# Performance work log

Hardware: AMD Instinct MI355X
Metric: run time of the kernel (lower is better)

The kernel has to match this reference:

```python
import jax, jax.numpy as jnp
import numpy as np

N_NODES, N_EDGES, N_GRAPHS, EMB_DIM, IMG_DIM, N_TYPES = 50000, 800000, 64, 128, 4096, 30


def gcn_conv(x, W, b, row, col, ew, dis, n):
    # PyG GCNConv: x @ W.T, symmetric-normalized weighted aggregation with self-loops, + bias
    xw = x @ W.T                                            # [N, D]
    norm = dis[row] * ew * dis[col]                          # [E]
    agg = jax.ops.segment_sum(norm[:, None] * xw[row], col, num_segments=n)
    agg = agg + (dis * dis)[:, None] * xw                    # self-loop (weight 1) term
    return agg + b


def setup_inputs() -> dict:
    key = jax.random.key(0)
    ks = jax.random.split(key, 20)
    inp = {
        "images": jax.random.normal(ks[0], (N_GRAPHS, IMG_DIM), jnp.float32),
        "node_types": jax.random.randint(ks[1], (N_NODES,), 0, N_TYPES),
        "edge_index": jax.random.randint(ks[2], (2, N_EDGES), 0, N_NODES),
        "edge_attr": jax.random.uniform(ks[3], (N_EDGES,), jnp.float32),
        "batch": jnp.sort(jax.random.randint(ks[4], (N_NODES,), 0, N_GRAPHS)),
    }
    def lin(k, out_d, in_d):
        s = 1.0 / np.sqrt(in_d)
        kw, kb = jax.random.split(k)
        return (jax.random.uniform(kw, (out_d, in_d), jnp.float32, -s, s),
                jax.random.uniform(kb, (out_d,), jnp.float32, -s, s))
    inp["emb_table"] = jax.random.normal(ks[5], (N_TYPES, EMB_DIM), jnp.float32)
    inp["W_img"], inp["b_img"] = lin(ks[6], IMG_DIM, IMG_DIM)      # frozen image backbone head
    inp["W1"], inp["b1"] = lin(ks[7], EMB_DIM, EMB_DIM)
    inp["W2"], inp["b2"] = lin(ks[8], EMB_DIM, EMB_DIM)
    inp["W3"], inp["b3"] = lin(ks[9], EMB_DIM, EMB_DIM)
    inp["Wi"], inp["bi"] = lin(ks[10], EMB_DIM, IMG_DIM)
    inp["Wc"], inp["bc"] = lin(ks[11], EMB_DIM, IMG_DIM + EMB_DIM)
    return inp


def reference(images, node_types, edge_index, edge_attr, batch, emb_table,
              W_img, b_img, W1, b1, W2, b2, W3, b3, Wi, bi, Wc, bc):
    n = node_types.shape[0]
    B = images.shape[0]
    row, col = edge_index[0], edge_index[1]
    # gcn_norm with self-loops (fill value 1): deg at aggregation endpoint (col)
    deg = jax.ops.segment_sum(edge_attr, col, num_segments=n) + 1.0
    dis = jax.lax.rsqrt(deg)
    # frozen image model (linear stand-in for VGG fc head, output dim 4096)
    xi = images @ W_img.T + b_img                           # [B, 4096]
    # encode_images branch
    oi = xi @ Wi.T + bi
    oi = oi / jnp.linalg.norm(oi, axis=1, keepdims=True)
    # encode_images_with_graphs branch
    xg = emb_table[node_types]                              # [N, D]
    xg = jax.nn.relu(gcn_conv(xg, W1, b1, row, col, edge_attr, dis, n))
    xg = jax.nn.relu(gcn_conv(xg, W2, b2, row, col, edge_attr, dis, n))
    xg = gcn_conv(xg, W3, b3, row, col, edge_attr, dis, n)
    cnt = jax.ops.segment_sum(jnp.ones((n,), xg.dtype), batch, num_segments=B)
    pooled = jax.ops.segment_sum(xg, batch, num_segments=B) / jnp.maximum(cnt, 1.0)[:, None]
    oc = jnp.concatenate([xi, pooled], axis=1) @ Wc.T + bc
    oc = oc / jnp.linalg.norm(oc, axis=1, keepdims=True)
    return (oi, oc)
```

## Files before the change

kernel.cpp:

```cpp
#include <hip/hip_runtime.h>
#include <math.h>

#define NN 50000
#define NE 800000
#define NG 64
#define D 128
#define IMG 4096
#define NT 30
#define CAP 64

#define EBLK (NE / 256)
#define PBLK ((NT * D + 2 * D * 64) / 256)
#define CBLK (64 * IMG / 2 / 256)
#define GBLK ((NN + 63) / 64)
#define AGGBLK ((NN + 7) / 8)
#define KSPLIT 16
#define IMGHALF (64 * KSPLIT / 2)
#define IREDBLK (64 * IMG / 256)

typedef unsigned int uint;
typedef unsigned short ushort;
typedef __attribute__((ext_vector_type(8))) __bf16 bf16x8;
typedef __attribute__((ext_vector_type(4))) float f32x4;

__device__ __forceinline__ uint bf16rne(float f) {
  uint h = __float_as_uint(f);
  return (h + 0x7fffu + ((h >> 16) & 1u)) >> 16;
}
__device__ __forceinline__ uint pack2bf(float a, float b) {
  return bf16rne(a) | (bf16rne(b) << 16);
}
__device__ __forceinline__ float bflo(uint u) { return __uint_as_float(u << 16); }
__device__ __forceinline__ float bfhi(uint u) { return __uint_as_float(u & 0xffff0000u); }



__global__ __launch_bounds__(256) void setup_multi(
    const int* __restrict__ row, const int* __restrict__ col,
    const float* __restrict__ ew, int* __restrict__ cnt, int2* __restrict__ ebuf,
    const float* __restrict__ emb, const float* __restrict__ W1, float* __restrict__ embW,
    const float* __restrict__ W2, const float* __restrict__ W3,
    uint* __restrict__ Wbf2, uint* __restrict__ Wbf3,
    const float* __restrict__ images, uint* __restrict__ imgAbf,
    const int* __restrict__ batch, int* __restrict__ goff) {
  int b = blockIdx.x;
  if (b < EBLK) {
    int e = b * 256 + threadIdx.x;
    if (e < NE) {
      int c = col[e];
      int s = atomicAdd(&cnt[c], 1);
      if (s < CAP) ebuf[((size_t)c << 6) + s] = make_int2(row[e], __float_as_int(ew[e]));
    }
  } else if (b < EBLK + PBLK) {
    int tid = (b - EBLK) * 256 + threadIdx.x;
    if (tid < NT * D) {
      int tt = tid >> 7, nn2 = tid & 127;
      const float* ep = emb + (size_t)tt * D;
      const float* wp = W1 + (size_t)nn2 * D;
      float acc = 0.f;
      for (int k = 0; k < D; k += 4) {
        float4 evv = *(const float4*)(ep + k);
        float4 wvv = *(const float4*)(wp + k);
        acc += evv.x * wvv.x + evv.y * wvv.y + evv.z * wvv.z + evv.w * wvv.w;
      }
      embW[tid] = acc;
    } else if (tid < NT * D + D * 64) {
      int j = tid - NT * D;
      float2 v = ((const float2*)W2)[j];
      Wbf2[j] = pack2bf(v.x, v.y);
    } else {
      int j = tid - NT * D - D * 64;
      float2 v = ((const float2*)W3)[j];
      Wbf3[j] = pack2bf(v.x, v.y);
    }
  } else if (b < EBLK + PBLK + CBLK) {
    int idx = (b - EBLK - PBLK) * 256 + threadIdx.x;
    float2 v = ((const float2*)images)[idx];
    imgAbf[idx] = pack2bf(v.x, v.y);
  } else {
    int g = threadIdx.x;
    if (g <= NG) {
      int lo = 0, hi = NN;
      while (lo < hi) {
        int mid = (lo + hi) >> 1;
        if (batch[mid] < g) lo = mid + 1; else hi = mid;
      }
      goff[g] = lo;
    }
  }
}


__global__ __launch_bounds__(256) void node_dis(const int* __restrict__ cnt,
                                                const int2* __restrict__ ebuf,
                                                float* __restrict__ dis) {
  int lane = threadIdx.x & 63;
  int sub = lane >> 4, fl = lane & 15;
  int node = (blockIdx.x * 4 + (threadIdx.x >> 6)) * 4 + sub;
  if (node >= NN) return;
  int n = min(cnt[node], CAP);
  const int2* eb = ebuf + ((size_t)node << 6);
  float acc = 0.f;
  for (int j = fl; j < n; j += 16) acc += __int_as_float(eb[j].y);
  acc += __shfl_xor(acc, 8);
  acc += __shfl_xor(acc, 4);
  acc += __shfl_xor(acc, 2);
  acc += __shfl_xor(acc, 1);
  if (fl == 0) dis[node] = 1.0f / sqrtf(acc + 1.0f);
}


__global__ __launch_bounds__(512) void lay1_fused(const int* __restrict__ cnt,
                                                  const int2* __restrict__ ebuf,
                                                  const float* __restrict__ dis,
                                                  const int* __restrict__ types,
                                                  const float* __restrict__ embW,
                                                  const float* __restrict__ b1,
                                                  uint* __restrict__ outbf) {
  __shared__ float sE[NT * D];
  __shared__ float sB[D];
  int t = threadIdx.x;
  for (int i = t; i < NT * D; i += 512) sE[i] = embW[i];
  if (t < D) sB[t] = b1[t];
  __syncthreads();
  int wave = t >> 6, lane = t & 63;
  #pragma unroll
  for (int r = 0; r < 4; r++) {
    int node = blockIdx.x * 32 + wave * 4 + r;
    if (node >= NN) continue;
    float ax = sB[2 * lane], ay = sB[2 * lane + 1];
    int n = min(cnt[node], CAP);
    const int2* eb = ebuf + ((size_t)node << 6);
    float disc = dis[node];
    int idx = 0;
    for (; idx + 4 <= n; idx += 4) {
      int4 ra = *(const int4*)(eb + idx);
      int4 rb = *(const int4*)(eb + idx + 2);
      float n0 = dis[ra.x] * __int_as_float(ra.y) * disc;
      float n1 = dis[ra.z] * __int_as_float(ra.w) * disc;
      float n2 = dis[rb.x] * __int_as_float(rb.y) * disc;
      float n3 = dis[rb.z] * __int_as_float(rb.w) * disc;
      float2 e0 = *(const float2*)&sE[types[ra.x] * D + 2 * lane];
      float2 e1 = *(const float2*)&sE[types[ra.z] * D + 2 * lane];
      float2 e2 = *(const float2*)&sE[types[rb.x] * D + 2 * lane];
      float2 e3 = *(const float2*)&sE[types[rb.z] * D + 2 * lane];
      ax = fmaf(n0, e0.x, ax); ay = fmaf(n0, e0.y, ay);
      ax = fmaf(n1, e1.x, ax); ay = fmaf(n1, e1.y, ay);
      ax = fmaf(n2, e2.x, ax); ay = fmaf(n2, e2.y, ay);
      ax = fmaf(n3, e3.x, ax); ay = fmaf(n3, e3.y, ay);
    }
    for (; idx < n; idx++) {
      int2 rr = eb[idx];
      float nm = dis[rr.x] * __int_as_float(rr.y) * disc;
      float2 ev = *(const float2*)&sE[types[rr.x] * D + 2 * lane];
      ax = fmaf(nm, ev.x, ax);
      ay = fmaf(nm, ev.y, ay);
    }
    float dd = disc * disc;
    float2 es = *(const float2*)&sE[types[node] * D + 2 * lane];
    ax = fmaf(dd, es.x, ax);
    ay = fmaf(dd, es.y, ay);
    ax = fmaxf(ax, 0.f);
    ay = fmaxf(ay, 0.f);
    outbf[(size_t)node * 64 + lane] = pack2bf(ax, ay);
  }
}


__device__ __forceinline__ void node_gemm_body(const uint* __restrict__ Abf,
                                               const uint* __restrict__ Wbf,
                                               uint* __restrict__ outbf, int bx,
                                               ushort* __restrict__ tile) {
  int w = threadIdx.x >> 6, lane = threadIdx.x & 63;
  int quad = lane >> 4;
  int m0 = bx * 64 + w * 16;
  int mrow = m0 + (lane & 15);
  int arow = (mrow < NN) ? mrow : 0;
  uint4 afr[4];
  #pragma unroll
  for (int ks = 0; ks < 4; ks++)
    afr[ks] = *(const uint4*)(Abf + (size_t)arow * 64 + ks * 16 + quad * 4);
  f32x4 acc[8] = {};
  #pragma unroll
  for (int nt = 0; nt < 8; nt++) {
    int n = nt * 16 + (lane & 15);
    #pragma unroll
    for (int ks = 0; ks < 4; ks++) {
      union { uint4 u; bf16x8 v; } au, bu;
      au.u = afr[ks];
      bu.u = *(const uint4*)(Wbf + (size_t)n * 64 + ks * 16 + quad * 4);
      acc[nt] = __builtin_amdgcn_mfma_f32_16x16x32_bf16(au.v, bu.v, acc[nt], 0, 0, 0);
    }
  }
  ushort* tw = tile + w * 16 * 136;
  #pragma unroll
  for (int nt = 0; nt < 8; nt++)
    #pragma unroll
    for (int i = 0; i < 4; i++)
      tw[(quad * 4 + i) * 136 + nt * 16 + (lane & 15)] = (ushort)bf16rne(acc[nt][i]);
  __builtin_amdgcn_s_waitcnt(0);
  #pragma unroll
  for (int rep = 0; rep < 4; rep++) {
    int r = rep * 4 + quad;
    int j = lane & 15;
    int node = m0 + r;
    if (node < NN) {
      uint4 v = *(const uint4*)&tw[r * 136 + j * 8];
      *(uint4*)(outbf + (size_t)node * 64 + j * 4) = v;
    }
  }
}


__device__ __forceinline__ void img_mfma_body(const uint* __restrict__ Abf,
                                              const float* __restrict__ W,
                                              float* __restrict__ splitbuf, int bx, int by) {
  int wv = threadIdx.x >> 6, lane = threadIdx.x & 63;
  int quad = lane >> 4;
  int n = bx * 64 + wv * 16 + (lane & 15);
  int k0 = by * 256;
  f32x4 acc[4] = {{0.f, 0.f, 0.f, 0.f}, {0.f, 0.f, 0.f, 0.f},
                  {0.f, 0.f, 0.f, 0.f}, {0.f, 0.f, 0.f, 0.f}};
  const float* wp = W + (size_t)n * IMG + k0 + quad * 16;
  const uint* ap = Abf + (size_t)(lane & 15) * (IMG / 2) + k0 / 2 + quad * 8;
  #pragma unroll
  for (int ss = 0; ss < 4; ss++) {
    float4 w0 = *(const float4*)(wp + ss * 64);
    float4 w1 = *(const float4*)(wp + ss * 64 + 4);
    float4 w2 = *(const float4*)(wp + ss * 64 + 8);
    float4 w3 = *(const float4*)(wp + ss * 64 + 12);
    union { uint4 u; bf16x8 v; } b1u, b2u;
    b1u.u.x = pack2bf(w0.x, w0.y);
    b1u.u.y = pack2bf(w0.z, w0.w);
    b1u.u.z = pack2bf(w1.x, w1.y);
    b1u.u.w = pack2bf(w1.z, w1.w);
    b2u.u.x = pack2bf(w2.x, w2.y);
    b2u.u.y = pack2bf(w2.z, w2.w);
    b2u.u.z = pack2bf(w3.x, w3.y);
    b2u.u.w = pack2bf(w3.z, w3.w);
    #pragma unroll
    for (int mt = 0; mt < 4; mt++) {
      const uint* app = ap + (size_t)mt * 16 * (IMG / 2) + ss * 32;
      union { uint4 u; bf16x8 v; } a1u, a2u;
      a1u.u = *(const uint4*)(app);
      a2u.u = *(const uint4*)(app + 4);
      acc[mt] = __builtin_amdgcn_mfma_f32_16x16x32_bf16(a1u.v, b1u.v, acc[mt], 0, 0, 0);
      acc[mt] = __builtin_amdgcn_mfma_f32_16x16x32_bf16(a2u.v, b2u.v, acc[mt], 0, 0, 0);
    }
  }
  #pragma unroll
  for (int mt = 0; mt < 4; mt++)
    #pragma unroll
    for (int i = 0; i < 4; i++) {
      int m = mt * 16 + quad * 4 + i;
      splitbuf[((size_t)by * 64 + m) * IMG + n] = acc[mt][i];
    }
}


__device__ __forceinline__ void aggregate2_body(const uint* __restrict__ xw,
                                                const int* __restrict__ cnt,
                                                const int2* __restrict__ ebuf,
                                                const float* __restrict__ dis,
                                                const float* __restrict__ bias, int relu,
                                                uint* __restrict__ outbf, int blk) {
  const uint2* xw2 = (const uint2*)xw;
  int wave = threadIdx.x >> 6;
  int lane = threadIdx.x & 63;
  int half = lane >> 5;
  int fl = lane & 31;
  int node = (blk * 4 + wave) * 2 + half;
  if (node >= NN) return;
  float a0 = 0.f, a1 = 0.f, a2 = 0.f, a3 = 0.f;
  int n = min(cnt[node], CAP);
  const int2* eb = ebuf + ((size_t)node << 6);
  float disc = dis[node];
  int idx = 0;
  for (; idx + 8 <= n; idx += 8) {
    int4 ra = *(const int4*)(eb + idx);
    int4 rb = *(const int4*)(eb + idx + 2);
    int4 rc = *(const int4*)(eb + idx + 4);
    int4 rd = *(const int4*)(eb + idx + 6);
    float n0 = dis[ra.x] * __int_as_float(ra.y) * disc;
    float n1 = dis[ra.z] * __int_as_float(ra.w) * disc;
    float n2 = dis[rb.x] * __int_as_float(rb.y) * disc;
    float n3 = dis[rb.z] * __int_as_float(rb.w) * disc;
    float n4 = dis[rc.x] * __int_as_float(rc.y) * disc;
    float n5 = dis[rc.z] * __int_as_float(rc.w) * disc;
    float n6 = dis[rd.x] * __int_as_float(rd.y) * disc;
    float n7 = dis[rd.z] * __int_as_float(rd.w) * disc;
    uint2 u0 = xw2[(size_t)ra.x * 32 + fl];
    uint2 u1 = xw2[(size_t)ra.z * 32 + fl];
    uint2 u2 = xw2[(size_t)rb.x * 32 + fl];
    uint2 u3 = xw2[(size_t)rb.z * 32 + fl];
    uint2 u4 = xw2[(size_t)rc.x * 32 + fl];
    uint2 u5 = xw2[(size_t)rc.z * 32 + fl];
    uint2 u6 = xw2[(size_t)rd.x * 32 + fl];
    uint2 u7 = xw2[(size_t)rd.z * 32 + fl];
    a0 = fmaf(n0, bflo(u0.x), a0); a1 = fmaf(n0, bfhi(u0.x), a1);
    a2 = fmaf(n0, bflo(u0.y), a2); a3 = fmaf(n0, bfhi(u0.y), a3);
    a0 = fmaf(n1, bflo(u1.x), a0); a1 = fmaf(n1, bfhi(u1.x), a1);
    a2 = fmaf(n1, bflo(u1.y), a2); a3 = fmaf(n1, bfhi(u1.y), a3);
    a0 = fmaf(n2, bflo(u2.x), a0); a1 = fmaf(n2, bfhi(u2.x), a1);
    a2 = fmaf(n2, bflo(u2.y), a2); a3 = fmaf(n2, bfhi(u2.y), a3);
    a0 = fmaf(n3, bflo(u3.x), a0); a1 = fmaf(n3, bfhi(u3.x), a1);
    a2 = fmaf(n3, bflo(u3.y), a2); a3 = fmaf(n3, bfhi(u3.y), a3);
    a0 = fmaf(n4, bflo(u4.x), a0); a1 = fmaf(n4, bfhi(u4.x), a1);
    a2 = fmaf(n4, bflo(u4.y), a2); a3 = fmaf(n4, bfhi(u4.y), a3);
    a0 = fmaf(n5, bflo(u5.x), a0); a1 = fmaf(n5, bfhi(u5.x), a1);
    a2 = fmaf(n5, bflo(u5.y), a2); a3 = fmaf(n5, bfhi(u5.y), a3);
    a0 = fmaf(n6, bflo(u6.x), a0); a1 = fmaf(n6, bfhi(u6.x), a1);
    a2 = fmaf(n6, bflo(u6.y), a2); a3 = fmaf(n6, bfhi(u6.y), a3);
    a0 = fmaf(n7, bflo(u7.x), a0); a1 = fmaf(n7, bfhi(u7.x), a1);
    a2 = fmaf(n7, bflo(u7.y), a2); a3 = fmaf(n7, bfhi(u7.y), a3);
  }
  for (; idx + 2 <= n; idx += 2) {
    int4 ra = *(const int4*)(eb + idx);
    float n0 = dis[ra.x] * __int_as_float(ra.y) * disc;
    float n1 = dis[ra.z] * __int_as_float(ra.w) * disc;
    uint2 u0 = xw2[(size_t)ra.x * 32 + fl];
    uint2 u1 = xw2[(size_t)ra.z * 32 + fl];
    a0 = fmaf(n0, bflo(u0.x), a0); a1 = fmaf(n0, bfhi(u0.x), a1);
    a2 = fmaf(n0, bflo(u0.y), a2); a3 = fmaf(n0, bfhi(u0.y), a3);
    a0 = fmaf(n1, bflo(u1.x), a0); a1 = fmaf(n1, bfhi(u1.x), a1);
    a2 = fmaf(n1, bflo(u1.y), a2); a3 = fmaf(n1, bfhi(u1.y), a3);
  }
  if (idx < n) {
    int2 r = eb[idx];
    float nm = dis[r.x] * __int_as_float(r.y) * disc;
    uint2 u = xw2[(size_t)r.x * 32 + fl];
    a0 = fmaf(nm, bflo(u.x), a0);
    a1 = fmaf(nm, bfhi(u.x), a1);
    a2 = fmaf(nm, bflo(u.y), a2);
    a3 = fmaf(nm, bfhi(u.y), a3);
  }
  float dd = disc * disc;
  {
    uint2 u = xw2[(size_t)node * 32 + fl];
    a0 = fmaf(dd, bflo(u.x), a0);
    a1 = fmaf(dd, bfhi(u.x), a1);
    a2 = fmaf(dd, bflo(u.y), a2);
    a3 = fmaf(dd, bfhi(u.y), a3);
  }
  float4 b = *(const float4*)(bias + 4 * fl);
  a0 += b.x; a1 += b.y; a2 += b.z; a3 += b.w;
  if (relu) {
    a0 = fmaxf(a0, 0.f);
    a1 = fmaxf(a1, 0.f);
    a2 = fmaxf(a2, 0.f);
    a3 = fmaxf(a3, 0.f);
  }
  uint2 o;
  o.x = pack2bf(a0, a1);
  o.y = pack2bf(a2, a3);
  ((uint2*)outbf)[(size_t)node * 32 + fl] = o;
}

__global__ __launch_bounds__(256) void gemm2_plus_img(const uint* __restrict__ bufX,
                                                      const uint* __restrict__ wbf2,
                                                      uint* __restrict__ bufB,
                                                      const uint* __restrict__ imgAbf,
                                                      const float* __restrict__ Wimg,
                                                      float* __restrict__ splitbuf) {
  __shared__ ushort tile[4 * 16 * 136];
  int b = blockIdx.x;
  if (b < GBLK) {
    node_gemm_body(bufX, wbf2, bufB, b, tile);
  } else {
    int j = b - GBLK;
    img_mfma_body(imgAbf, Wimg, splitbuf, j & 63, j >> 6);
  }
}

__global__ __launch_bounds__(256) void agg2_plus_img(const uint* __restrict__ bufB,
                                                     const int* __restrict__ cnt,
                                                     const int2* __restrict__ ebuf,
                                                     const float* __restrict__ dis,
                                                     const float* __restrict__ b2,
                                                     uint* __restrict__ bufX,
                                                     const uint* __restrict__ imgAbf,
                                                     const float* __restrict__ Wimg,
                                                     float* __restrict__ splitbuf) {
  int b = blockIdx.x;
  if (b < AGGBLK) {
    aggregate2_body(bufB, cnt, ebuf, dis, b2, 1, bufX, b);
  } else {
    int j = b - AGGBLK;
    img_mfma_body(imgAbf, Wimg, splitbuf, j & 63, 8 + (j >> 6));
  }
}

__global__ __launch_bounds__(256) void gemm3_plus_imgred(const uint* __restrict__ bufX,
                                                         const uint* __restrict__ wbf3,
                                                         uint* __restrict__ bufB,
                                                         const float* __restrict__ splitbuf,
                                                         const float* __restrict__ b_img,
                                                         float* __restrict__ xcat) {
  __shared__ ushort tile[4 * 16 * 136];
  int b = blockIdx.x;
  if (b < GBLK) {
    node_gemm_body(bufX, wbf3, bufB, b, tile);
  } else {
    int idx = (b - GBLK) * 256 + threadIdx.x;
    if (idx < 64 * IMG) {
      float acc = b_img[idx & (IMG - 1)];
      #pragma unroll
      for (int s = 0; s < KSPLIT; s++) acc += splitbuf[(size_t)s * 64 * IMG + idx];
      xcat[(size_t)(idx >> 12) * (IMG + D) + (idx & (IMG - 1))] = acc;
    }
  }
}

__global__ __launch_bounds__(256) void aggregate2(const uint* __restrict__ xw,
                                                  const int* __restrict__ cnt,
                                                  const int2* __restrict__ ebuf,
                                                  const float* __restrict__ dis,
                                                  const float* __restrict__ bias, int relu,
                                                  uint* __restrict__ outbf) {
  aggregate2_body(xw, cnt, ebuf, dis, bias, relu, outbf, blockIdx.x);
}


__device__ __forceinline__ void gemm64_body(const float* __restrict__ A, int lda,
                                            const float* __restrict__ W,
                                            const float* __restrict__ bias,
                                            float* __restrict__ out, int N, int K,
                                            int kChunk, int bx, int by,
                                            float (*xs)[68], float (*ws)[68]) {
  int t = threadIdx.x;
  int n0 = bx * 64;
  int k0 = by * kChunk;
  int kEnd = min(K, k0 + kChunk);
  int tn = t & 15;
  int tm = t >> 4;
  float acc[4][4] = {};
  if (by == 0) {
    #pragma unroll
    for (int ni = 0; ni < 4; ni++) {
      float bv = bias[n0 + tn * 4 + ni];
      #pragma unroll
      for (int mi = 0; mi < 4; mi++) acc[mi][ni] = bv;
    }
  }
  for (int kt = k0; kt < kEnd; kt += 16) {
    int kc = (t & 3) * 4;
    int rr = t >> 2;
    float4 va = *(const float4*)(A + (size_t)rr * lda + kt + kc);
    xs[kc + 0][rr] = va.x; xs[kc + 1][rr] = va.y; xs[kc + 2][rr] = va.z; xs[kc + 3][rr] = va.w;
    float4 vw = *(const float4*)(W + (size_t)(n0 + rr) * K + kt + kc);
    ws[kc + 0][rr] = vw.x; ws[kc + 1][rr] = vw.y; ws[kc + 2][rr] = vw.z; ws[kc + 3][rr] = vw.w;
    __syncthreads();
    #pragma unroll
    for (int k = 0; k < 16; k++) {
      float4 xv = *(const float4*)&xs[k][tm * 4];
      float4 wv = *(const float4*)&ws[k][tn * 4];
      float xm[4] = {xv.x, xv.y, xv.z, xv.w};
      float wn[4] = {wv.x, wv.y, wv.z, wv.w};
      #pragma unroll
      for (int mi = 0; mi < 4; mi++)
        #pragma unroll
        for (int ni = 0; ni < 4; ni++)
          acc[mi][ni] = fmaf(xm[mi], wn[ni], acc[mi][ni]);
    }
    __syncthreads();
  }
  #pragma unroll
  for (int mi = 0; mi < 4; mi++)
    #pragma unroll
    for (int ni = 0; ni < 4; ni++)
      atomicAdd(&out[(size_t)(tm * 4 + mi) * N + n0 + tn * 4 + ni], acc[mi][ni]);
}


__global__ __launch_bounds__(256) void pool_gemm_oi(const uint* __restrict__ xb,
                                                    const int* __restrict__ goff,
                                                    float* __restrict__ xcat,
                                                    const float* __restrict__ Wi,
                                                    const float* __restrict__ bi,
                                                    float* __restrict__ oi_raw) {
  __shared__ float xs[16][68];
  __shared__ float ws[16][68];
  int b = blockIdx.x;
  if (b < 2 * NG) {
    int g = b >> 1;
    int chunk = ((b & 1) << 2) + (threadIdx.x >> 6);
    int fl = threadIdx.x & 63;
    int s = goff[g], e = goff[g + 1];
    float inv = 1.0f / fmaxf((float)(e - s), 1.0f);
    float ax = 0.f, ay = 0.f;
    for (int i = s + chunk; i < e; i += 8) {
      uint u = xb[(size_t)i * 64 + fl];
      ax += bflo(u);
      ay += bfhi(u);
    }
    atomicAdd(&xcat[(size_t)g * (IMG + D) + IMG + 2 * fl], ax * inv);
    atomicAdd(&xcat[(size_t)g * (IMG + D) + IMG + 2 * fl + 1], ay * inv);
  } else {
    int j = b - 2 * NG;
    gemm64_body(xcat, IMG + D, Wi, bi, oi_raw, D, IMG, 128, j & 1, j >> 1, xs, ws);
  }
}

__global__ __launch_bounds__(256) void gemm_oc(const float* __restrict__ xcat,
                                               const float* __restrict__ Wc,
                                               const float* __restrict__ bc,
                                               float* __restrict__ oc_raw) {
  __shared__ float xs[16][68];
  __shared__ float ws[16][68];
  int b = blockIdx.x;
  gemm64_body(xcat, IMG + D, Wc, bc, oc_raw, D, IMG + D, 176, b & 1, b >> 1, xs, ws);
}

__global__ __launch_bounds__(128) void normalize_rows(const float* __restrict__ oi_raw,
                                                      const float* __restrict__ oc_raw,
                                                      float* __restrict__ out) {
  int r = blockIdx.x;
  int t = threadIdx.x;
  const float* src = (r < 64) ? (oi_raw + r * D) : (oc_raw + (r - 64) * D);
  float v = src[t];
  __shared__ float red[128];
  red[t] = v * v;
  __syncthreads();
  for (int s = 64; s > 0; s >>= 1) {
    if (t < s) red[t] += red[t + s];
    __syncthreads();
  }
  out[r * D + t] = v / sqrtf(red[0]);
}


extern "C" void kernel_launch(void* const* d_in, const int* in_sizes, int n_in,
                              void* d_out, int out_size, void* d_ws, size_t ws_size,
                              hipStream_t stream) {
  const float* images = (const float*)d_in[0];
  const int* node_types = (const int*)d_in[1];
  const int* erow = (const int*)d_in[2];
  const int* ecol = erow + NE;
  const float* eattr = (const float*)d_in[3];
  const int* batch = (const int*)d_in[4];
  const float* emb = (const float*)d_in[5];
  const float* W_img = (const float*)d_in[6];
  const float* b_img = (const float*)d_in[7];
  const float* W1 = (const float*)d_in[8];
  const float* b1 = (const float*)d_in[9];
  const float* W2 = (const float*)d_in[10];
  const float* b2 = (const float*)d_in[11];
  const float* W3 = (const float*)d_in[12];
  const float* b3 = (const float*)d_in[13];
  const float* Wi = (const float*)d_in[14];
  const float* bi = (const float*)d_in[15];
  const float* Wc = (const float*)d_in[16];
  const float* bc = (const float*)d_in[17];
  float* out = (float*)d_out;

  char* w = (char*)d_ws;
  auto alloc = [&](size_t bytes) -> void* {
    void* p = (void*)w;
    w += (bytes + 511) & ~(size_t)511;
    return p;
  };
  int* cnt = (int*)alloc((size_t)NN * 4);
  float* xcat = (float*)alloc((size_t)64 * (IMG + D) * 4);
  float* oi_raw = (float*)alloc(64 * D * 4);
  float* oc_raw = (float*)alloc(64 * D * 4);
  size_t zero_bytes = (size_t)(w - (char*)d_ws);
  int* goff = (int*)alloc((NG + 1) * 4);
  float* dis = (float*)alloc(NN * 4);
  float* embW1 = (float*)alloc(NT * D * 4);
  uint* wbf2 = (uint*)alloc(D * 64 * 4);
  uint* wbf3 = (uint*)alloc(D * 64 * 4);
  int2* ebuf = (int2*)alloc((size_t)NN * CAP * 8);
  uint* bufX = (uint*)alloc((size_t)NN * D * 2);
  uint* bufB = (uint*)alloc((size_t)NN * D * 2);
  uint* imgAbf = (uint*)alloc((size_t)64 * IMG * 2);
  float* splitbuf = (float*)alloc((size_t)KSPLIT * 64 * IMG * 4);

  hipMemsetAsync(d_ws, 0, zero_bytes, stream);

  setup_multi<<<EBLK + PBLK + CBLK + 1, 256, 0, stream>>>(
      erow, ecol, eattr, cnt, ebuf, emb, W1, embW1, W2, W3, wbf2, wbf3,
      images, imgAbf, batch, goff);
  node_dis<<<(NN + 15) / 16, 256, 0, stream>>>(cnt, ebuf, dis);
  lay1_fused<<<(NN + 31) / 32, 512, 0, stream>>>(cnt, ebuf, dis, node_types, embW1, b1, bufX);
  gemm2_plus_img<<<GBLK + IMGHALF, 256, 0, stream>>>(bufX, wbf2, bufB, imgAbf, W_img,
                                                     splitbuf);
  agg2_plus_img<<<AGGBLK + IMGHALF, 256, 0, stream>>>(bufB, cnt, ebuf, dis, b2, bufX,
                                                      imgAbf, W_img, splitbuf);
  gemm3_plus_imgred<<<GBLK + IREDBLK, 256, 0, stream>>>(bufX, wbf3, bufB, splitbuf, b_img,
                                                        xcat);
  aggregate2<<<AGGBLK, 256, 0, stream>>>(bufB, cnt, ebuf, dis, b3, 0, bufX);
  pool_gemm_oi<<<2 * NG + 64, 256, 0, stream>>>(bufX, goff, xcat, Wi, bi, oi_raw);
  gemm_oc<<<48, 256, 0, stream>>>(xcat, Wc, bc, oc_raw);
  normalize_rows<<<128, 128, 0, stream>>>(oi_raw, oc_raw, out);
}
```

Measured before the change: 422.6 us.

## Zero-pad edge buckets, atomic degree, reorder fused blocks, split pooling kernel

Degree is now accumulated with float atomics during bucketing, which replaces the per-node reduction kernel with a trivial rsqrt kernel. The edge bucket capacity drops to 48 and the buffer is zeroed, so the aggregation loops can run in fixed 8- or 16-edge chunks with no tail handling. Padded entries point to node 0 with weight zero and contribute nothing. The fused kernels now put the image GEMM blocks first so they are scheduled ahead of the graph blocks. The layer-3 aggregation is fused with the oi GEMM, and pooling moves to its own wider kernel. The cost is a larger memset, extra atomics, and truncation for nodes with more than 48 in-edges, which changes results when such nodes exist.

```diff
diff --git a/kernel.cpp b/kernel.cpp
--- a/kernel.cpp
+++ b/kernel.cpp
@@ -7,7 +7,7 @@
 #define D 128
 #define IMG 4096
 #define NT 30
-#define CAP 64
+#define CAP 48
 
 #define EBLK (NE / 256)
 #define PBLK ((NT * D + 2 * D * 64) / 256)
@@ -37,7 +37,8 @@
 
 __global__ __launch_bounds__(256) void setup_multi(
     const int* __restrict__ row, const int* __restrict__ col,
-    const float* __restrict__ ew, int* __restrict__ cnt, int2* __restrict__ ebuf,
+    const float* __restrict__ ew, int* __restrict__ cnt, float* __restrict__ degf,
+    int2* __restrict__ ebuf,
     const float* __restrict__ emb, const float* __restrict__ W1, float* __restrict__ embW,
     const float* __restrict__ W2, const float* __restrict__ W3,
     uint* __restrict__ Wbf2, uint* __restrict__ Wbf3,
@@ -48,8 +49,10 @@
     int e = b * 256 + threadIdx.x;
     if (e < NE) {
       int c = col[e];
+      float wv = ew[e];
       int s = atomicAdd(&cnt[c], 1);
-      if (s < CAP) ebuf[((size_t)c << 6) + s] = make_int2(row[e], __float_as_int(ew[e]));
+      atomicAdd(&degf[c], wv);
+      if (s < CAP) ebuf[(size_t)c * CAP + s] = make_int2(row[e], __float_as_int(wv));
     }
   } else if (b < EBLK + PBLK) {
     int tid = (b - EBLK) * 256 + threadIdx.x;
@@ -91,22 +94,10 @@
 }
 
 
-__global__ __launch_bounds__(256) void node_dis(const int* __restrict__ cnt,
-                                                const int2* __restrict__ ebuf,
-                                                float* __restrict__ dis) {
-  int lane = threadIdx.x & 63;
-  int sub = lane >> 4, fl = lane & 15;
-  int node = (blockIdx.x * 4 + (threadIdx.x >> 6)) * 4 + sub;
-  if (node >= NN) return;
-  int n = min(cnt[node], CAP);
-  const int2* eb = ebuf + ((size_t)node << 6);
-  float acc = 0.f;
-  for (int j = fl; j < n; j += 16) acc += __int_as_float(eb[j].y);
-  acc += __shfl_xor(acc, 8);
-  acc += __shfl_xor(acc, 4);
-  acc += __shfl_xor(acc, 2);
-  acc += __shfl_xor(acc, 1);
-  if (fl == 0) dis[node] = 1.0f / sqrtf(acc + 1.0f);
+__global__ __launch_bounds__(256) void dis_kernel(const float* __restrict__ degf,
+                                                  float* __restrict__ dis) {
+  int i = blockIdx.x * 256 + threadIdx.x;
+  if (i < NN) dis[i] = 1.0f / sqrtf(degf[i] + 1.0f);
 }
 
 
@@ -130,31 +121,41 @@
     if (node >= NN) continue;
     float ax = sB[2 * lane], ay = sB[2 * lane + 1];
     int n = min(cnt[node], CAP);
-    const int2* eb = ebuf + ((size_t)node << 6);
+    int nc = (n + 7) >> 3;
+    const int2* eb = ebuf + (size_t)node * CAP;
     float disc = dis[node];
-    int idx = 0;
-    for (; idx + 4 <= n; idx += 4) {
-      int4 ra = *(const int4*)(eb + idx);
-      int4 rb = *(const int4*)(eb + idx + 2);
-      float n0 = dis[ra.x] * __int_as_float(ra.y) * disc;
-      float n1 = dis[ra.z] * __int_as_float(ra.w) * disc;
-      float n2 = dis[rb.x] * __int_as_float(rb.y) * disc;
-      float n3 = dis[rb.z] * __int_as_float(rb.w) * disc;
-      float2 e0 = *(const float2*)&sE[types[ra.x] * D + 2 * lane];
-      float2 e1 = *(const float2*)&sE[types[ra.z] * D + 2 * lane];
-      float2 e2 = *(const float2*)&sE[types[rb.x] * D + 2 * lane];
-      float2 e3 = *(const float2*)&sE[types[rb.z] * D + 2 * lane];
-      ax = fmaf(n0, e0.x, ax); ay = fmaf(n0, e0.y, ay);
-      ax = fmaf(n1, e1.x, ax); ay = fmaf(n1, e1.y, ay);
-      ax = fmaf(n2, e2.x, ax); ay = fmaf(n2, e2.y, ay);
-      ax = fmaf(n3, e3.x, ax); ay = fmaf(n3, e3.y, ay);
-    }
-    for (; idx < n; idx++) {
-      int2 rr = eb[idx];
-      float nm = dis[rr.x] * __int_as_float(rr.y) * disc;
-      float2 ev = *(const float2*)&sE[types[rr.x] * D + 2 * lane];
-      ax = fmaf(nm, ev.x, ax);
-      ay = fmaf(nm, ev.y, ay);
+    for (int c = 0; c < nc; c++) {
+      const int2* ep = eb + (c << 3);
+      int4 q0 = *(const int4*)(ep + 0);
+      int4 q1 = *(const int4*)(ep + 2);
+      int4 q2 = *(const int4*)(ep + 4);
+      int4 q3 = *(const int4*)(ep + 6);
+      int t0 = types[q0.x], t1 = types[q0.z], t2 = types[q1.x], t3 = types[q1.z];
+      int t4 = types[q2.x], t5 = types[q2.z], t6 = types[q3.x], t7 = types[q3.z];
+      float m0 = dis[q0.x] * __int_as_float(q0.y) * disc;
+      float m1 = dis[q0.z] * __int_as_float(q0.w) * disc;
+      float m2 = dis[q1.x] * __int_as_float(q1.y) * disc;
+      float m3 = dis[q1.z] * __int_as_float(q1.w) * disc;
+      float m4 = dis[q2.x] * __int_as_float(q2.y) * disc;
+      float m5 = dis[q2.z] * __int_as_float(q2.w) * disc;
+      float m6 = dis[q3.x] * __int_as_float(q3.y) * disc;
+      float m7 = dis[q3.z] * __int_as_float(q3.w) * disc;
+      float2 e0 = *(const float2*)&sE[t0 * D + 2 * lane];
+      float2 e1 = *(const float2*)&sE[t1 * D + 2 * lane];
+      float2 e2 = *(const float2*)&sE[t2 * D + 2 * lane];
+      float2 e3 = *(const float2*)&sE[t3 * D + 2 * lane];
+      float2 e4 = *(const float2*)&sE[t4 * D + 2 * lane];
+      float2 e5 = *(const float2*)&sE[t5 * D + 2 * lane];
+      float2 e6 = *(const float2*)&sE[t6 * D + 2 * lane];
+      float2 e7 = *(const float2*)&sE[t7 * D + 2 * lane];
+      ax = fmaf(m0, e0.x, ax); ay = fmaf(m0, e0.y, ay);
+      ax = fmaf(m1, e1.x, ax); ay = fmaf(m1, e1.y, ay);
+      ax = fmaf(m2, e2.x, ax); ay = fmaf(m2, e2.y, ay);
+      ax = fmaf(m3, e3.x, ax); ay = fmaf(m3, e3.y, ay);
+      ax = fmaf(m4, e4.x, ax); ay = fmaf(m4, e4.y, ay);
+      ax = fmaf(m5, e5.x, ax); ay = fmaf(m5, e5.y, ay);
+      ax = fmaf(m6, e6.x, ax); ay = fmaf(m6, e6.y, ay);
+      ax = fmaf(m7, e7.x, ax); ay = fmaf(m7, e7.y, ay);
     }
     float dd = disc * disc;
     float2 es = *(const float2*)&sE[types[node] * D + 2 * lane];
@@ -257,6 +258,10 @@
     }
 }
 
+
+#define GA(k, s_) uint2 u##k = xw2[(size_t)(s_) * 32 + fl];
+#define FA(k, m_) a0 = fmaf(m_, bflo(u##k.x), a0); a1 = fmaf(m_, bfhi(u##k.x), a1); \
+                  a2 = fmaf(m_, bflo(u##k.y), a2); a3 = fmaf(m_, bfhi(u##k.y), a3);
 
 __device__ __forceinline__ void aggregate2_body(const uint* __restrict__ xw,
                                                 const int* __restrict__ cnt,
@@ -273,66 +278,43 @@
   if (node >= NN) return;
   float a0 = 0.f, a1 = 0.f, a2 = 0.f, a3 = 0.f;
   int n = min(cnt[node], CAP);
-  const int2* eb = ebuf + ((size_t)node << 6);
+  int nc = (n + 15) >> 4;
+  const int2* eb = ebuf + (size_t)node * CAP;
   float disc = dis[node];
-  int idx = 0;
-  for (; idx + 8 <= n; idx += 8) {
-    int4 ra = *(const int4*)(eb + idx);
-    int4 rb = *(const int4*)(eb + idx + 2);
-    int4 rc = *(const int4*)(eb + idx + 4);
-    int4 rd = *(const int4*)(eb + idx + 6);
-    float n0 = dis[ra.x] * __int_as_float(ra.y) * disc;
-    float n1 = dis[ra.z] * __int_as_float(ra.w) * disc;
-    float n2 = dis[rb.x] * __int_as_float(rb.y) * disc;
-    float n3 = dis[rb.z] * __int_as_float(rb.w) * disc;
-    float n4 = dis[rc.x] * __int_as_float(rc.y) * disc;
-    float n5 = dis[rc.z] * __int_as_float(rc.w) * disc;
-    float n6 = dis[rd.x] * __int_as_float(rd.y) * disc;
-    float n7 = dis[rd.z] * __int_as_float(rd.w) * disc;
-    uint2 u0 = xw2[(size_t)ra.x * 32 + fl];
-    uint2 u1 = xw2[(size_t)ra.z * 32 + fl];
-    uint2 u2 = xw2[(size_t)rb.x * 32 + fl];
-    uint2 u3 = xw2[(size_t)rb.z * 32 + fl];
-    uint2 u4 = xw2[(size_t)rc.x * 32 + fl];
-    uint2 u5 = xw2[(size_t)rc.z * 32 + fl];
-    uint2 u6 = xw2[(size_t)rd.x * 32 + fl];
-    uint2 u7 = xw2[(size_t)rd.z * 32 + fl];
-    a0 = fmaf(n0, bflo(u0.x), a0); a1 = fmaf(n0, bfhi(u0.x), a1);
-    a2 = fmaf(n0, bflo(u0.y), a2); a3 = fmaf(n0, bfhi(u0.y), a3);
-    a0 = fmaf(n1, bflo(u1.x), a0); a1 = fmaf(n1, bfhi(u1.x), a1);
-    a2 = fmaf(n1, bflo(u1.y), a2); a3 = fmaf(n1, bfhi(u1.y), a3);
-    a0 = fmaf(n2, bflo(u2.x), a0); a1 = fmaf(n2, bfhi(u2.x), a1);
-    a2 = fmaf(n2, bflo(u2.y), a2); a3 = fmaf(n2, bfhi(u2.y), a3);
-    a0 = fmaf(n3, bflo(u3.x), a0); a1 = fmaf(n3, bfhi(u3.x), a1);
-    a2 = fmaf(n3, bflo(u3.y), a2); a3 = fmaf(n3, bfhi(u3.y), a3);
-    a0 = fmaf(n4, bflo(u4.x), a0); a1 = fmaf(n4, bfhi(u4.x), a1);
-    a2 = fmaf(n4, bflo(u4.y), a2); a3 = fmaf(n4, bfhi(u4.y), a3);
-    a0 = fmaf(n5, bflo(u5.x), a0); a1 = fmaf(n5, bfhi(u5.x), a1);
-    a2 = fmaf(n5, bflo(u5.y), a2); a3 = fmaf(n5, bfhi(u5.y), a3);
-    a0 = fmaf(n6, bflo(u6.x), a0); a1 = fmaf(n6, bfhi(u6.x), a1);
-    a2 = fmaf(n6, bflo(u6.y), a2); a3 = fmaf(n6, bfhi(u6.y), a3);
-    a0 = fmaf(n7, bflo(u7.x), a0); a1 = fmaf(n7, bfhi(u7.x), a1);
-    a2 = fmaf(n7, bflo(u7.y), a2); a3 = fmaf(n7, bfhi(u7.y), a3);
-  }
-  for (; idx + 2 <= n; idx += 2) {
-    int4 ra = *(const int4*)(eb + idx);
-    float n0 = dis[ra.x] * __int_as_float(ra.y) * disc;
-    float n1 = dis[ra.z] * __int_as_float(ra.w) * disc;
-    uint2 u0 = xw2[(size_t)ra.x * 32 + fl];
-    uint2 u1 = xw2[(size_t)ra.z * 32 + fl];
-    a0 = fmaf(n0, bflo(u0.x), a0); a1 = fmaf(n0, bfhi(u0.x), a1);
-    a2 = fmaf(n0, bflo(u0.y), a2); a3 = fmaf(n0, bfhi(u0.y), a3);
-    a0 = fmaf(n1, bflo(u1.x), a0); a1 = fmaf(n1, bfhi(u1.x), a1);
-    a2 = fmaf(n1, bflo(u1.y), a2); a3 = fmaf(n1, bfhi(u1.y), a3);
-  }
-  if (idx < n) {
-    int2 r = eb[idx];
-    float nm = dis[r.x] * __int_as_float(r.y) * disc;
-    uint2 u = xw2[(size_t)r.x * 32 + fl];
-    a0 = fmaf(nm, bflo(u.x), a0);
-    a1 = fmaf(nm, bfhi(u.x), a1);
-    a2 = fmaf(nm, bflo(u.y), a2);
-    a3 = fmaf(nm, bfhi(u.y), a3);
+  for (int c = 0; c < nc; c++) {
+    const int2* ep = eb + (c << 4);
+    int4 r0 = *(const int4*)(ep + 0);
+    int4 r1 = *(const int4*)(ep + 2);
+    int4 r2 = *(const int4*)(ep + 4);
+    int4 r3 = *(const int4*)(ep + 6);
+    int4 r4 = *(const int4*)(ep + 8);
+    int4 r5 = *(const int4*)(ep + 10);
+    int4 r6 = *(const int4*)(ep + 12);
+    int4 r7 = *(const int4*)(ep + 14);
+    GA(0, r0.x)  GA(1, r0.z)  GA(2, r1.x)  GA(3, r1.z)
+    GA(4, r2.x)  GA(5, r2.z)  GA(6, r3.x)  GA(7, r3.z)
+    GA(8, r4.x)  GA(9, r4.z)  GA(10, r5.x) GA(11, r5.z)
+    GA(12, r6.x) GA(13, r6.z) GA(14, r7.x) GA(15, r7.z)
+    float m0 = dis[r0.x] * __int_as_float(r0.y) * disc;
+    float m1 = dis[r0.z] * __int_as_float(r0.w) * disc;
+    float m2 = dis[r1.x] * __int_as_float(r1.y) * disc;
+    float m3 = dis[r1.z] * __int_as_float(r1.w) * disc;
+    float m4 = dis[r2.x] * __int_as_float(r2.y) * disc;
+    float m5 = dis[r2.z] * __int_as_float(r2.w) * disc;
+    float m6 = dis[r3.x] * __int_as_float(r3.y) * disc;
+    float m7 = dis[r3.z] * __int_as_float(r3.w) * disc;
+    float m8 = dis[r4.x] * __int_as_float(r4.y) * disc;
+    float m9 = dis[r4.z] * __int_as_float(r4.w) * disc;
+    float m10 = dis[r5.x] * __int_as_float(r5.y) * disc;
+    float m11 = dis[r5.z] * __int_as_float(r5.w) * disc;
+    float m12 = dis[r6.x] * __int_as_float(r6.y) * disc;
+    float m13 = dis[r6.z] * __int_as_float(r6.w) * disc;
+    float m14 = dis[r7.x] * __int_as_float(r7.y) * disc;
+    float m15 = dis[r7.z] * __int_as_float(r7.w) * disc;
+    FA(0, m0)  FA(1, m1)  FA(2, m2)  FA(3, m3)
+    FA(4, m4)  FA(5, m5)  FA(6, m6)  FA(7, m7)
+    FA(8, m8)  FA(9, m9)  FA(10, m10) FA(11, m11)
+    FA(12, m12) FA(13, m13) FA(14, m14) FA(15, m15)
   }
   float dd = disc * disc;
   {
@@ -364,11 +346,10 @@
                                                       float* __restrict__ splitbuf) {
   __shared__ ushort tile[4 * 16 * 136];
   int b = blockIdx.x;
-  if (b < GBLK) {
-    node_gemm_body(bufX, wbf2, bufB, b, tile);
+  if (b < IMGHALF) {
+    img_mfma_body(imgAbf, Wimg, splitbuf, b & 63, b >> 6);
   } else {
-    int j = b - GBLK;
-    img_mfma_body(imgAbf, Wimg, splitbuf, j & 63, j >> 6);
+    node_gemm_body(bufX, wbf2, bufB, b - IMGHALF, tile);
   }
 }
 
@@ -382,11 +363,10 @@
                                                      const float* __restrict__ Wimg,
                                                      float* __restrict__ splitbuf) {
   int b = blockIdx.x;
-  if (b < AGGBLK) {
-    aggregate2_body(bufB, cnt, ebuf, dis, b2, 1, bufX, b);
+  if (b < IMGHALF) {
+    img_mfma_body(imgAbf, Wimg, splitbuf, b & 63, 8 + (b >> 6));
   } else {
-    int j = b - AGGBLK;
-    img_mfma_body(imgAbf, Wimg, splitbuf, j & 63, 8 + (j >> 6));
+    aggregate2_body(bufB, cnt, ebuf, dis, b2, 1, bufX, b - IMGHALF);
   }
 }
 
@@ -398,26 +378,15 @@
                                                          float* __restrict__ xcat) {
   __shared__ ushort tile[4 * 16 * 136];
   int b = blockIdx.x;
-  if (b < GBLK) {
-    node_gemm_body(bufX, wbf3, bufB, b, tile);
+  if (b < IREDBLK) {
+    int idx = b * 256 + threadIdx.x;
+    float acc = b_img[idx & (IMG - 1)];
+    #pragma unroll
+    for (int s = 0; s < KSPLIT; s++) acc += splitbuf[(size_t)s * 64 * IMG + idx];
+    xcat[(size_t)(idx >> 12) * (IMG + D) + (idx & (IMG - 1))] = acc;
   } else {
-    int idx = (b - GBLK) * 256 + threadIdx.x;
-    if (idx < 64 * IMG) {
-      float acc = b_img[idx & (IMG - 1)];
-      #pragma unroll
-      for (int s = 0; s < KSPLIT; s++) acc += splitbuf[(size_t)s * 64 * IMG + idx];
-      xcat[(size_t)(idx >> 12) * (IMG + D) + (idx & (IMG - 1))] = acc;
-    }
-  }
-}
-
-__global__ __launch_bounds__(256) void aggregate2(const uint* __restrict__ xw,
-                                                  const int* __restrict__ cnt,
-                                                  const int2* __restrict__ ebuf,
-                                                  const float* __restrict__ dis,
-                                                  const float* __restrict__ bias, int relu,
-                                                  uint* __restrict__ outbf) {
-  aggregate2_body(xw, cnt, ebuf, dis, bias, relu, outbf, blockIdx.x);
+    node_gemm_body(bufX, wbf3, bufB, b - IREDBLK, tile);
+  }
 }
 
 
@@ -471,34 +440,43 @@
       atomicAdd(&out[(size_t)(tm * 4 + mi) * N + n0 + tn * 4 + ni], acc[mi][ni]);
 }
 
-
-__global__ __launch_bounds__(256) void pool_gemm_oi(const uint* __restrict__ xb,
-                                                    const int* __restrict__ goff,
-                                                    float* __restrict__ xcat,
+__global__ __launch_bounds__(256) void agg3_plus_oi(const uint* __restrict__ bufB,
+                                                    const int* __restrict__ cnt,
+                                                    const int2* __restrict__ ebuf,
+                                                    const float* __restrict__ dis,
+                                                    const float* __restrict__ b3,
+                                                    uint* __restrict__ bufX,
+                                                    const float* __restrict__ xcat,
                                                     const float* __restrict__ Wi,
                                                     const float* __restrict__ bi,
                                                     float* __restrict__ oi_raw) {
   __shared__ float xs[16][68];
   __shared__ float ws[16][68];
   int b = blockIdx.x;
-  if (b < 2 * NG) {
-    int g = b >> 1;
-    int chunk = ((b & 1) << 2) + (threadIdx.x >> 6);
-    int fl = threadIdx.x & 63;
-    int s = goff[g], e = goff[g + 1];
-    float inv = 1.0f / fmaxf((float)(e - s), 1.0f);
-    float ax = 0.f, ay = 0.f;
-    for (int i = s + chunk; i < e; i += 8) {
-      uint u = xb[(size_t)i * 64 + fl];
-      ax += bflo(u);
-      ay += bfhi(u);
-    }
-    atomicAdd(&xcat[(size_t)g * (IMG + D) + IMG + 2 * fl], ax * inv);
-    atomicAdd(&xcat[(size_t)g * (IMG + D) + IMG + 2 * fl + 1], ay * inv);
+  if (b < 64) {
+    gemm64_body(xcat, IMG + D, Wi, bi, oi_raw, D, IMG, 128, b & 1, b >> 1, xs, ws);
   } else {
-    int j = b - 2 * NG;
-    gemm64_body(xcat, IMG + D, Wi, bi, oi_raw, D, IMG, 128, j & 1, j >> 1, xs, ws);
-  }
+    aggregate2_body(bufB, cnt, ebuf, dis, b3, 0, bufX, b - 64);
+  }
+}
+
+
+__global__ __launch_bounds__(64) void pool_bf(const uint* __restrict__ xb,
+                                              const int* __restrict__ goff,
+                                              float* __restrict__ xcat) {
+  int g = blockIdx.x >> 5;
+  int chunk = blockIdx.x & 31;
+  int fl = threadIdx.x;
+  int s = goff[g], e = goff[g + 1];
+  float inv = 1.0f / fmaxf((float)(e - s), 1.0f);
+  float ax = 0.f, ay = 0.f;
+  for (int i = s + chunk; i < e; i += 32) {
+    uint u = xb[(size_t)i * 64 + fl];
+    ax += bflo(u);
+    ay += bfhi(u);
+  }
+  atomicAdd(&xcat[(size_t)g * (IMG + D) + IMG + 2 * fl], ax * inv);
+  atomicAdd(&xcat[(size_t)g * (IMG + D) + IMG + 2 * fl + 1], ay * inv);
 }
 
 __global__ __launch_bounds__(256) void gemm_oc(const float* __restrict__ xcat,
@@ -560,16 +538,17 @@
     return p;
   };
   int* cnt = (int*)alloc((size_t)NN * 4);
+  float* degf = (float*)alloc((size_t)NN * 4);
   float* xcat = (float*)alloc((size_t)64 * (IMG + D) * 4);
   float* oi_raw = (float*)alloc(64 * D * 4);
   float* oc_raw = (float*)alloc(64 * D * 4);
+  int2* ebuf = (int2*)alloc((size_t)NN * CAP * 8);
   size_t zero_bytes = (size_t)(w - (char*)d_ws);
   int* goff = (int*)alloc((NG + 1) * 4);
   float* dis = (float*)alloc(NN * 4);
   float* embW1 = (float*)alloc(NT * D * 4);
   uint* wbf2 = (uint*)alloc(D * 64 * 4);
   uint* wbf3 = (uint*)alloc(D * 64 * 4);
-  int2* ebuf = (int2*)alloc((size_t)NN * CAP * 8);
   uint* bufX = (uint*)alloc((size_t)NN * D * 2);
   uint* bufB = (uint*)alloc((size_t)NN * D * 2);
   uint* imgAbf = (uint*)alloc((size_t)64 * IMG * 2);
@@ -578,18 +557,19 @@
   hipMemsetAsync(d_ws, 0, zero_bytes, stream);
 
   setup_multi<<<EBLK + PBLK + CBLK + 1, 256, 0, stream>>>(
-      erow, ecol, eattr, cnt, ebuf, emb, W1, embW1, W2, W3, wbf2, wbf3,
+      erow, ecol, eattr, cnt, degf, ebuf, emb, W1, embW1, W2, W3, wbf2, wbf3,
       images, imgAbf, batch, goff);
-  node_dis<<<(NN + 15) / 16, 256, 0, stream>>>(cnt, ebuf, dis);
+  dis_kernel<<<(NN + 255) / 256, 256, 0, stream>>>(degf, dis);
   lay1_fused<<<(NN + 31) / 32, 512, 0, stream>>>(cnt, ebuf, dis, node_types, embW1, b1, bufX);
-  gemm2_plus_img<<<GBLK + IMGHALF, 256, 0, stream>>>(bufX, wbf2, bufB, imgAbf, W_img,
+  gemm2_plus_img<<<IMGHALF + GBLK, 256, 0, stream>>>(bufX, wbf2, bufB, imgAbf, W_img,
                                                      splitbuf);
-  agg2_plus_img<<<AGGBLK + IMGHALF, 256, 0, stream>>>(bufB, cnt, ebuf, dis, b2, bufX,
+  agg2_plus_img<<<IMGHALF + AGGBLK, 256, 0, stream>>>(bufB, cnt, ebuf, dis, b2, bufX,
                                                       imgAbf, W_img, splitbuf);
-  gemm3_plus_imgred<<<GBLK + IREDBLK, 256, 0, stream>>>(bufX, wbf3, bufB, splitbuf, b_img,
+  gemm3_plus_imgred<<<IREDBLK + GBLK, 256, 0, stream>>>(bufX, wbf3, bufB, splitbuf, b_img,
                                                         xcat);
-  aggregate2<<<AGGBLK, 256, 0, stream>>>(bufB, cnt, ebuf, dis, b3, 0, bufX);
-  pool_gemm_oi<<<2 * NG + 64, 256, 0, stream>>>(bufX, goff, xcat, Wi, bi, oi_raw);
+  agg3_plus_oi<<<64 + AGGBLK, 256, 0, stream>>>(bufB, cnt, ebuf, dis, b3, bufX,
+                                                xcat, Wi, bi, oi_raw);
+  pool_bf<<<NG * 32, 64, 0, stream>>>(bufX, goff, xcat);
   gemm_oc<<<48, 256, 0, stream>>>(xcat, Wc, bc, oc_raw);
   normalize_rows<<<128, 128, 0, stream>>>(oi_raw, oc_raw, out);
 }
```

New measurement: 443.3 us. +4.9%, slower.
